# Performance work log

Measured on AMD Instinct MI355X. Metric: run time of the kernel, lower is better.

The kernel has to match this reference:

```python
import jax, jax.numpy as jnp
import numpy as np

SCALE = 0.125  # 1/sqrt(d_head=64)

def setup_inputs() -> dict:
    key = jax.random.key(0)
    kq, kk, kv = jax.random.split(key, 3)
    shape = (2, 12, 2048, 64)  # [batch, heads, seq, d_head]
    q = jax.random.normal(kq, shape, dtype=jnp.float32)
    k = jax.random.normal(kk, shape, dtype=jnp.float32)
    v = jax.random.normal(kv, shape, dtype=jnp.float32)
    return {"q": q, "k": k, "v": v}

def reference(q, k, v) -> jnp.ndarray:
    # atten = softmax(q @ k^T * scale); res = atten @ v
    scores = jnp.einsum('bhik,bhjk->bhij', q, k) * SCALE  # [B,H,S,S]
    atten = jax.nn.softmax(scores, axis=-1)
    # dropout is Identity (atten_dropout=None)
    res = jnp.einsum('bhij,bhjd->bhid', atten, v)  # [B,H,S,D]
    return res
```

## Files before the change

### kernel.cpp

```cpp
#include <hip/hip_runtime.h>
#include <math.h>

#define SEQ   2048
#define DH    64
#define NBH   24
#define QSCALE 0.18033688011112042f

typedef __attribute__((ext_vector_type(8))) short short8;
typedef __attribute__((ext_vector_type(4))) short short4v;
typedef __attribute__((ext_vector_type(4))) float f32x4;

#define MFMA32(a, b, c) __builtin_amdgcn_mfma_f32_16x16x32_bf16((a), (b), (c), 0, 0, 0)
#define MFMA16(a, b, c) __builtin_amdgcn_mfma_f32_16x16x16bf16_1k((a), (b), (c), 0, 0, 0)

__device__ __forceinline__ int cvtpk(float lo, float hi) {
    int r;
    asm("v_cvt_pk_bf16_f32 %0, %1, %2" : "=v"(r) : "v"(lo), "v"(hi));
    return r;
}

__global__ __launch_bounds__(256)
void cvt_all(const float* __restrict__ q, const float* __restrict__ k,
             const float* __restrict__ v,
             short* __restrict__ qb, short* __restrict__ kb,
             short* __restrict__ vt)
{
    __shared__ float tile[32][68];
    const int t  = threadIdx.x;
    const int bh = blockIdx.x;
    const int s0 = blockIdx.y * 32;
    const size_t base = ((size_t)bh * SEQ + s0) * DH;
    const size_t kbh  = (size_t)bh * SEQ * DH;

    #pragma unroll
    for (int i = 0; i < 2; ++i) {
        const int idx = i * 256 + t;
        float4 a = ((const float4*)(q + base))[idx];
        ((int2*)(qb + base))[idx] = make_int2(
            cvtpk(a.x * QSCALE, a.y * QSCALE),
            cvtpk(a.z * QSCALE, a.w * QSCALE));

        float4 b = ((const float4*)(k + base))[idx];
        {
            const int sl   = idx >> 4;
            const int fgrp = idx & 15;
            const int sblk = (s0 >> 4) + (sl >> 4);
            const int half = fgrp >> 3;
            const int quad = (fgrp >> 1) & 3;
            const int r04  = (fgrp & 1) * 4;
            short* p = kb + kbh + (size_t)sblk * 1024 + half * 512
                     + (quad * 16 + (sl & 15)) * 8 + r04;
            *(int2*)p = make_int2(cvtpk(b.x, b.y), cvtpk(b.z, b.w));
        }

        float4 c = ((const float4*)(v + base))[idx];
        const int sl = idx >> 4, cg = (idx & 15) * 4;
        *(float4*)(&tile[sl][cg]) = c;
    }
    __syncthreads();
    {
        const int dl = t >> 2;
        const int qq = t & 3;
        float f[8];
        #pragma unroll
        for (int r = 0; r < 4; ++r) {
            f[r]     = tile[qq * 4 + r][dl];
            f[4 + r] = tile[16 + qq * 4 + r][dl];
        }
        short8 pc;
        ((int*)&pc)[0] = cvtpk(f[0], f[1]);
        ((int*)&pc)[1] = cvtpk(f[2], f[3]);
        ((int*)&pc)[2] = cvtpk(f[4], f[5]);
        ((int*)&pc)[3] = cvtpk(f[6], f[7]);
        short* p = vt + kbh + (size_t)((s0 >> 5) * 4 + (dl >> 4)) * 512
                 + (qq * 16 + (dl & 15)) * 8;
        *(short8*)p = pc;
    }
}

__global__ __launch_bounds__(256, 3)
void attn_fwd(const short* __restrict__ qb, const short* __restrict__ kb,
              const short* __restrict__ vt, float* __restrict__ og)
{
    const int lane = threadIdx.x & 63;
    const int wave = threadIdx.x >> 6;
    const int quad = lane >> 4;
    const int l16  = lane & 15;
    const int lane8 = lane * 8;

    const int swz = (blockIdx.x & 7) * 48 + (blockIdx.x >> 3);
    const int bh  = swz >> 4;
    const int q0  = (swz & 15) * 128 + wave * 32;

    const short* kbase = kb + (size_t)bh * SEQ * DH;
    const short* vbase = vt + (size_t)bh * DH * SEQ;

    short8 bq[2][2];
    #pragma unroll
    for (int qs = 0; qs < 2; ++qs) {
        const short* qrow = qb + ((size_t)(bh * SEQ + q0 + qs * 16 + l16)) * DH + quad * 8;
        bq[qs][0] = *(const short8*)(qrow);
        bq[qs][1] = *(const short8*)(qrow + 32);
    }

    f32x4 o[2][4];
    float l_i[2];
    #pragma unroll
    for (int qs = 0; qs < 2; ++qs) {
        l_i[qs] = 0.f;
        #pragma unroll
        for (int dt = 0; dt < 4; ++dt) o[qs][dt] = (f32x4){0.f, 0.f, 0.f, 0.f};
    }

    int k0 = 0;
    short8 ka[8];
    #pragma unroll
    for (int mt = 0; mt < 4; ++mt) {
        const short* kc = kbase + (size_t)mt * 1024 + lane8;
        ka[2 * mt]     = *(const short8*)(kc);
        ka[2 * mt + 1] = *(const short8*)(kc + 512);
    }

    #pragma unroll 1
    for (int iter = 0; iter < 32; ++iter, k0 += 64) {
        __builtin_amdgcn_s_barrier();

        short8 av[2][4];
        #pragma unroll
        for (int pair = 0; pair < 2; ++pair)
            #pragma unroll
            for (int dt = 0; dt < 4; ++dt)
                av[pair][dt] = *(const short8*)(vbase
                    + (size_t)((((k0 >> 5) + pair) * 4) + dt) * 512 + lane8);

        short4v pb[2][4];

        #pragma unroll
        for (int qs = 0; qs < 2; ++qs) {
            f32x4 c[4];
            __builtin_amdgcn_s_setprio(1);
            #pragma unroll
            for (int mt = 0; mt < 4; ++mt) {
                f32x4 z = (f32x4){0.f, 0.f, 0.f, 0.f};
                z = MFMA32(ka[2 * mt],     bq[qs][0], z);
                z = MFMA32(ka[2 * mt + 1], bq[qs][1], z);
                c[mt] = z;
            }
            __builtin_amdgcn_s_setprio(0);

            if (qs == 1 && iter < 31) {
                const int k0n = k0 + 64;
                #pragma unroll
                for (int mt = 0; mt < 4; ++mt) {
                    const short* kc = kbase + (size_t)((k0n >> 4) + mt) * 1024 + lane8;
                    ka[2 * mt]     = *(const short8*)(kc);
                    ka[2 * mt + 1] = *(const short8*)(kc + 512);
                }
            }

            float rsm[4];
            #pragma unroll
            for (int mt = 0; mt < 4; ++mt) {
                float p[4];
                #pragma unroll
                for (int r = 0; r < 4; ++r)
                    p[r] = __builtin_amdgcn_exp2f(c[mt][r]);
                rsm[mt] = (p[0] + p[1]) + (p[2] + p[3]);
                int2 w = make_int2(cvtpk(p[0], p[1]), cvtpk(p[2], p[3]));
                pb[qs][mt] = __builtin_bit_cast(short4v, w);
            }
            l_i[qs] += (rsm[0] + rsm[1]) + (rsm[2] + rsm[3]);
        }

        __builtin_amdgcn_s_setprio(1);
        #pragma unroll
        for (int pair = 0; pair < 2; ++pair) {
            #pragma unroll
            for (int dt = 0; dt < 4; ++dt) {
                const short4v alo = __builtin_shufflevector(av[pair][dt], av[pair][dt], 0, 1, 2, 3);
                const short4v ahi = __builtin_shufflevector(av[pair][dt], av[pair][dt], 4, 5, 6, 7);
                #pragma unroll
                for (int qs = 0; qs < 2; ++qs) {
                    o[qs][dt] = MFMA16(alo, pb[qs][2 * pair],     o[qs][dt]);
                    o[qs][dt] = MFMA16(ahi, pb[qs][2 * pair + 1], o[qs][dt]);
                }
            }
        }
        __builtin_amdgcn_s_setprio(0);
    }

    #pragma unroll
    for (int qs = 0; qs < 2; ++qs) {
        float l = l_i[qs];
        l += __shfl_xor(l, 16, 64);
        l += __shfl_xor(l, 32, 64);
        const float linv = 1.0f / l;
        float* orow = og + ((size_t)(bh * SEQ + q0 + qs * 16 + l16)) * DH;
        #pragma unroll
        for (int dt = 0; dt < 4; ++dt) {
            f32x4 st;
            #pragma unroll
            for (int r = 0; r < 4; ++r) st[r] = o[qs][dt][r] * linv;
            *(f32x4*)(orow + dt * 16 + quad * 4) = st;
        }
    }
}

extern "C" void kernel_launch(void* const* d_in, const int* in_sizes, int n_in,
                              void* d_out, int out_size, void* d_ws, size_t ws_size,
                              hipStream_t stream)
{
    const float* q = (const float*)d_in[0];
    const float* k = (const float*)d_in[1];
    const float* v = (const float*)d_in[2];
    float* o = (float*)d_out;

    const size_t nelem = (size_t)NBH * SEQ * DH;
    short* qb  = (short*)d_ws;
    short* kbp = qb + nelem;
    short* vtp = kbp + nelem;

    cvt_all<<<dim3(NBH, SEQ / 32), 256, 0, stream>>>(q, k, v, qb, kbp, vtp);
    attn_fwd<<<dim3(NBH * (SEQ / 128) * (128 / 128) * 16 / 16), 256, 0, stream>>>(qb, kbp, vtp, o);
}
```

Before: 136.2 us.

## Stage K/V tiles in LDS via async global_load_lds double-buffering with 2-wave blocks

Each block now has two waves covering 64 query rows. K and V tiles are staged into double-buffered LDS with direct global-to-LDS loads, one wave loading K and the other V, and each wave reads its operands from LDS. This replaces per-wave redundant register loads from global memory and is meant to cut L2 traffic and hide load latency. The PV MFMAs are also interleaved per query subtile, and the launch bounds move to 128 threads. The cost is 32KB of LDS per block, a __syncthreads every iteration, half the K/V reuse per block compared with 4 waves, and twice as many blocks.

```diff
diff --git a/kernel.cpp b/kernel.cpp
--- a/kernel.cpp
+++ b/kernel.cpp
@@ -12,6 +12,11 @@
 
 #define MFMA32(a, b, c) __builtin_amdgcn_mfma_f32_16x16x32_bf16((a), (b), (c), 0, 0, 0)
 #define MFMA16(a, b, c) __builtin_amdgcn_mfma_f32_16x16x16bf16_1k((a), (b), (c), 0, 0, 0)
+
+#define GLOAD_LDS(g, l) \
+    __builtin_amdgcn_global_load_lds( \
+        (const __attribute__((address_space(1))) void*)(const void*)(g), \
+        (__attribute__((address_space(3))) void*)(void*)(l), 16, 0, 0)
 
 __device__ __forceinline__ int cvtpk(float lo, float hi) {
     int r;
@@ -78,19 +83,22 @@
     }
 }
 
-__global__ __launch_bounds__(256, 3)
+__global__ __launch_bounds__(128, 2)
 void attn_fwd(const short* __restrict__ qb, const short* __restrict__ kb,
               const short* __restrict__ vt, float* __restrict__ og)
 {
-    const int lane = threadIdx.x & 63;
-    const int wave = threadIdx.x >> 6;
-    const int quad = lane >> 4;
-    const int l16  = lane & 15;
+    __shared__ short ldsK[2][4096];
+    __shared__ short ldsV[2][4096];
+
+    const int lane  = threadIdx.x & 63;
+    const int wave  = threadIdx.x >> 6;
+    const int quad  = lane >> 4;
+    const int l16   = lane & 15;
     const int lane8 = lane * 8;
 
-    const int swz = (blockIdx.x & 7) * 48 + (blockIdx.x >> 3);
-    const int bh  = swz >> 4;
-    const int q0  = (swz & 15) * 128 + wave * 32;
+    const int swz = (blockIdx.x & 7) * 96 + (blockIdx.x >> 3);
+    const int bh  = swz >> 5;
+    const int q0  = (swz & 31) * 64 + wave * 32;
 
     const short* kbase = kb + (size_t)bh * SEQ * DH;
     const short* vbase = vt + (size_t)bh * DH * SEQ;
@@ -112,28 +120,50 @@
         for (int dt = 0; dt < 4; ++dt) o[qs][dt] = (f32x4){0.f, 0.f, 0.f, 0.f};
     }
 
-    int k0 = 0;
-    short8 ka[8];
-    #pragma unroll
-    for (int mt = 0; mt < 4; ++mt) {
-        const short* kc = kbase + (size_t)mt * 1024 + lane8;
-        ka[2 * mt]     = *(const short8*)(kc);
-        ka[2 * mt + 1] = *(const short8*)(kc + 512);
-    }
-
+    if (wave == 0) {
+        const short* src = kbase + lane8;
+        #pragma unroll
+        for (int j = 0; j < 8; ++j)
+            GLOAD_LDS(src + j * 512, &ldsK[0][j * 512]);
+    } else {
+        const short* src = vbase + lane8;
+        #pragma unroll
+        for (int j = 0; j < 8; ++j)
+            GLOAD_LDS(src + j * 512, &ldsV[0][j * 512]);
+    }
+    __syncthreads();
+
+    int cur = 0;
     #pragma unroll 1
-    for (int iter = 0; iter < 32; ++iter, k0 += 64) {
-        __builtin_amdgcn_s_barrier();
-
-        short8 av[2][4];
+    for (int iter = 0; iter < 32; ++iter) {
+        const int k0 = iter * 64;
+
+        if (iter < 31) {
+            const int k0n = k0 + 64;
+            if (wave == 0) {
+                const short* src = kbase + (size_t)(k0n >> 4) * 1024 + lane8;
+                #pragma unroll
+                for (int j = 0; j < 8; ++j)
+                    GLOAD_LDS(src + j * 512, &ldsK[cur ^ 1][j * 512]);
+            } else {
+                const short* src = vbase + (size_t)(k0n >> 5) * 2048 + lane8;
+                #pragma unroll
+                for (int j = 0; j < 8; ++j)
+                    GLOAD_LDS(src + j * 512, &ldsV[cur ^ 1][j * 512]);
+            }
+        }
+
+        short8 ka[8], av[2][4];
+        #pragma unroll
+        for (int mt = 0; mt < 4; ++mt) {
+            ka[2 * mt]     = *(const short8*)&ldsK[cur][mt * 1024 + lane8];
+            ka[2 * mt + 1] = *(const short8*)&ldsK[cur][mt * 1024 + 512 + lane8];
+        }
         #pragma unroll
         for (int pair = 0; pair < 2; ++pair)
             #pragma unroll
             for (int dt = 0; dt < 4; ++dt)
-                av[pair][dt] = *(const short8*)(vbase
-                    + (size_t)((((k0 >> 5) + pair) * 4) + dt) * 512 + lane8);
-
-        short4v pb[2][4];
+                av[pair][dt] = *(const short8*)&ldsV[cur][(pair * 4 + dt) * 512 + lane8];
 
         #pragma unroll
         for (int qs = 0; qs < 2; ++qs) {
@@ -148,16 +178,7 @@
             }
             __builtin_amdgcn_s_setprio(0);
 
-            if (qs == 1 && iter < 31) {
-                const int k0n = k0 + 64;
-                #pragma unroll
-                for (int mt = 0; mt < 4; ++mt) {
-                    const short* kc = kbase + (size_t)((k0n >> 4) + mt) * 1024 + lane8;
-                    ka[2 * mt]     = *(const short8*)(kc);
-                    ka[2 * mt + 1] = *(const short8*)(kc + 512);
-                }
-            }
-
+            short4v pb[4];
             float rsm[4];
             #pragma unroll
             for (int mt = 0; mt < 4; ++mt) {
@@ -167,26 +188,26 @@
                     p[r] = __builtin_amdgcn_exp2f(c[mt][r]);
                 rsm[mt] = (p[0] + p[1]) + (p[2] + p[3]);
                 int2 w = make_int2(cvtpk(p[0], p[1]), cvtpk(p[2], p[3]));
-                pb[qs][mt] = __builtin_bit_cast(short4v, w);
+                pb[mt] = __builtin_bit_cast(short4v, w);
             }
             l_i[qs] += (rsm[0] + rsm[1]) + (rsm[2] + rsm[3]);
-        }
-
-        __builtin_amdgcn_s_setprio(1);
-        #pragma unroll
-        for (int pair = 0; pair < 2; ++pair) {
-            #pragma unroll
-            for (int dt = 0; dt < 4; ++dt) {
-                const short4v alo = __builtin_shufflevector(av[pair][dt], av[pair][dt], 0, 1, 2, 3);
-                const short4v ahi = __builtin_shufflevector(av[pair][dt], av[pair][dt], 4, 5, 6, 7);
-                #pragma unroll
-                for (int qs = 0; qs < 2; ++qs) {
-                    o[qs][dt] = MFMA16(alo, pb[qs][2 * pair],     o[qs][dt]);
-                    o[qs][dt] = MFMA16(ahi, pb[qs][2 * pair + 1], o[qs][dt]);
+
+            __builtin_amdgcn_s_setprio(1);
+            #pragma unroll
+            for (int pair = 0; pair < 2; ++pair) {
+                #pragma unroll
+                for (int dt = 0; dt < 4; ++dt) {
+                    const short4v alo = __builtin_shufflevector(av[pair][dt], av[pair][dt], 0, 1, 2, 3);
+                    const short4v ahi = __builtin_shufflevector(av[pair][dt], av[pair][dt], 4, 5, 6, 7);
+                    o[qs][dt] = MFMA16(alo, pb[2 * pair],     o[qs][dt]);
+                    o[qs][dt] = MFMA16(ahi, pb[2 * pair + 1], o[qs][dt]);
                 }
             }
-        }
-        __builtin_amdgcn_s_setprio(0);
+            __builtin_amdgcn_s_setprio(0);
+        }
+
+        __syncthreads();
+        cur ^= 1;
     }
 
     #pragma unroll
@@ -221,5 +242,5 @@
     short* vtp = kbp + nelem;
 
     cvt_all<<<dim3(NBH, SEQ / 32), 256, 0, stream>>>(q, k, v, qb, kbp, vtp);
-    attn_fwd<<<dim3(NBH * (SEQ / 128) * (128 / 128) * 16 / 16), 256, 0, stream>>>(qb, kbp, vtp, o);
-}
+    attn_fwd<<<dim3(NBH * (SEQ / 64)), 128, 0, stream>>>(qb, kbp, vtp, o);
+}
```

Result: faster. 128.1 us (-5.9%).
